# Kernel tuning notes

Measured on AMD Instinct MI355X. Metric: run time of the kernel, lower is better.

The kernel has to match this reference:

```python
import jax, jax.numpy as jnp
import numpy as np

DIM = 1024
HEADS = 16
HEAD_DIM = DIM // HEADS
FFN = 4 * DIM
EPS = 1e-5


def layer_norm(x, g, b):
    mu = jnp.mean(x, axis=-1, keepdims=True)
    var = jnp.mean(jnp.square(x - mu), axis=-1, keepdims=True)
    return (x - mu) * jax.lax.rsqrt(var + EPS) * g + b


def setup_inputs() -> dict:
    key = jax.random.key(0)
    ks = jax.random.split(key, 12)
    s_d = 1.0 / np.sqrt(DIM)
    s_f = 1.0 / np.sqrt(FFN)
    return {
        "x": jax.random.normal(ks[0], (2, 2048, DIM), dtype=jnp.float32),
        "ln1_g": jnp.ones((DIM,), jnp.float32),
        "ln1_b": jnp.zeros((DIM,), jnp.float32),
        "q_w": jax.random.normal(ks[1], (DIM, DIM), jnp.float32) * s_d,
        "k_w": jax.random.normal(ks[2], (DIM, DIM), jnp.float32) * s_d,
        "v_w": jax.random.normal(ks[3], (DIM, DIM), jnp.float32) * s_d,
        "o_w": jax.random.normal(ks[4], (DIM, DIM), jnp.float32) * s_d,
        "ln2_g": jnp.ones((DIM,), jnp.float32),
        "ln2_b": jnp.zeros((DIM,), jnp.float32),
        "ffn_in_w": jax.random.normal(ks[5], (FFN, DIM), jnp.float32) * s_d,
        "ffn_in_b": jnp.zeros((FFN,), jnp.float32),
        "sw_w": jax.random.normal(ks[6], (FFN, FFN), jnp.float32) * s_f,
        "sw_v": jax.random.normal(ks[7], (FFN, FFN), jnp.float32) * s_f,
        "ffn_out_w": jax.random.normal(ks[8], (DIM, FFN), jnp.float32) * s_f,
        "ffn_out_b": jnp.zeros((DIM,), jnp.float32),
    }


def reference(x, ln1_g, ln1_b, q_w, k_w, v_w, o_w, ln2_g, ln2_b,
              ffn_in_w, ffn_in_b, sw_w, sw_v, ffn_out_w, ffn_out_b):
    B, L, D = x.shape
    scale = HEAD_DIM ** -0.5

    # --- attention block ---
    h = layer_norm(x, ln1_g, ln1_b)
    q = (h @ q_w.T).reshape(B, L, HEADS, HEAD_DIM).transpose(0, 2, 1, 3)
    k = (h @ k_w.T).reshape(B, L, HEADS, HEAD_DIM).transpose(0, 2, 1, 3)
    v = (h @ v_w.T).reshape(B, L, HEADS, HEAD_DIM).transpose(0, 2, 1, 3)
    attn = jnp.einsum("bhqd,bhkd->bhqk", q, k) * scale
    attn = jax.nn.softmax(attn, axis=-1)
    out = jnp.einsum("bhqk,bhkd->bhqd", attn, v)
    out = out.transpose(0, 2, 1, 3).reshape(B, L, D)
    x = x + out @ o_w.T

    # --- FFN block: Linear -> SwiGLU -> Linear ---
    h = layer_norm(x, ln2_g, ln2_b)
    u = h @ ffn_in_w.T + ffn_in_b                 # [B,L,FFN]
    g = jax.nn.silu(u @ sw_w.T) * (u @ sw_v.T)    # SwiGLU
    x = x + g @ ffn_out_w.T + ffn_out_b
    return x
```

## Files before the change

kernel.cpp:

```cpp
#include <hip/hip_runtime.h>
#include <hip/hip_bf16.h>

#define TOK 4096
#define DIM 1024
#define FFN_N 4096
#define SEQ 2048
#define HD 64

using short8 = __attribute__((ext_vector_type(8))) short;
using short4v = __attribute__((ext_vector_type(4))) short;
using f32x4 = __attribute__((ext_vector_type(4))) float;

__device__ __forceinline__ short f2b(float f){
  return __builtin_bit_cast(short, __float2bfloat16(f));
}
__device__ __forceinline__ float b2f(short s){
  return __bfloat162float(__builtin_bit_cast(__hip_bfloat16, s));
}
__device__ __forceinline__ unsigned cvtpk(float lo, float hi){
  unsigned r;
  asm("v_cvt_pk_bf16_f32 %0, %1, %2" : "=v"(r) : "v"(lo), "v"(hi));
  return r;
}

__device__ __forceinline__ void gl_lds16(const short* g, short* l){
  __builtin_amdgcn_global_load_lds(
      (const __attribute__((address_space(1))) unsigned int*)g,
      (__attribute__((address_space(3))) unsigned int*)l, 16, 0, 0);
}

#define BARRAW() asm volatile("s_barrier" ::: "memory")
#define VMCNT(n) asm volatile("s_waitcnt vmcnt(" #n ")" ::: "memory")

__global__ __launch_bounds__(256) void castk(const float* __restrict__ src,
                                             short* __restrict__ dst, int n){
  int stride = gridDim.x*256*4;
  for (int i = (blockIdx.x*256 + threadIdx.x)*4; i < n; i += stride){
    float4 v = *reinterpret_cast<const float4*>(src + i);
    short4v o; o[0]=f2b(v.x); o[1]=f2b(v.y); o[2]=f2b(v.z); o[3]=f2b(v.w);
    *reinterpret_cast<short4v*>(dst + i) = o;
  }
}

__global__ __launch_bounds__(256) void lnk(const float* __restrict__ x,
                                           const float* __restrict__ g,
                                           const float* __restrict__ b,
                                           short* __restrict__ out){
  int row = blockIdx.x;
  int t = threadIdx.x;
  const float* xr = x + (size_t)row*DIM;
  float4 v = *reinterpret_cast<const float4*>(xr + t*4);
  float s = v.x+v.y+v.z+v.w;
  float s2 = v.x*v.x+v.y*v.y+v.z*v.z+v.w*v.w;
  #pragma unroll
  for (int off=1; off<64; off<<=1){ s += __shfl_xor(s,off); s2 += __shfl_xor(s2,off); }
  __shared__ float as_[4], as2_[4];
  if ((t&63)==0){ as_[t>>6]=s; as2_[t>>6]=s2; }
  __syncthreads();
  s = as_[0]+as_[1]+as_[2]+as_[3];
  s2 = as2_[0]+as2_[1]+as2_[2]+as2_[3];
  float mu = s * (1.0f/DIM);
  float var = s2 * (1.0f/DIM) - mu*mu;
  float r = rsqrtf(var + 1e-5f);
  float4 gv = *reinterpret_cast<const float4*>(g + t*4);
  float4 bv = *reinterpret_cast<const float4*>(b + t*4);
  short4v o;
  o[0]=f2b((v.x-mu)*r*gv.x + bv.x);
  o[1]=f2b((v.y-mu)*r*gv.y + bv.y);
  o[2]=f2b((v.z-mu)*r*gv.z + bv.z);
  o[3]=f2b((v.w-mu)*r*gv.w + bv.w);
  *reinterpret_cast<short4v*>(out + (size_t)row*DIM + t*4) = o;
}

template<int MODE>
__global__ __launch_bounds__(256,2) void gemm_bt(
    const short* __restrict__ A, const short* __restrict__ Bt,
    short* __restrict__ Cb, float* __restrict__ Cf,
    const float* __restrict__ bias, const float* __restrict__ resid,
    const short* __restrict__ aux,
    int M, int N, int K)
{
  __shared__ __align__(16) short Al[128*32];
  __shared__ __align__(16) short Bl[128*32];
  const int tid = threadIdx.x, lane = tid & 63, w = tid >> 6;
  const int wr = w >> 1, wc = w & 1;
  const int bx = blockIdx.x, by = blockIdx.y;

  const short* ga0 = A  + (size_t)(by*128 + w*32 + (lane>>2))*K + (lane&3)*8;
  const short* gb0 = Bt + (size_t)(bx*128 + w*32 + (lane>>2))*K + (lane&3)*8;
  short* la0 = &Al[w*32*32];
  short* lb0 = &Bl[w*32*32];

  f32x4 acc[4][4] = {};

  for (int k0 = 0; k0 < K; k0 += 32){
    __syncthreads();
    gl_lds16(ga0 + k0,                 la0);
    gl_lds16(ga0 + k0 + (size_t)16*K,  la0 + 16*32);
    gl_lds16(gb0 + k0,                 lb0);
    gl_lds16(gb0 + k0 + (size_t)16*K,  lb0 + 16*32);
    __syncthreads();
    short8 af[4], bf[4];
    #pragma unroll
    for (int m=0;m<4;m++)
      af[m] = *reinterpret_cast<const short8*>(&Al[(wr*64 + m*16 + (lane&15))*32 + (lane>>4)*8]);
    #pragma unroll
    for (int n=0;n<4;n++)
      bf[n] = *reinterpret_cast<const short8*>(&Bl[(wc*64 + n*16 + (lane&15))*32 + (lane>>4)*8]);
    #pragma unroll
    for (int m=0;m<4;m++)
      #pragma unroll
      for (int n=0;n<4;n++)
        acc[m][n] = __builtin_amdgcn_mfma_f32_16x16x32_bf16(af[m], bf[n], acc[m][n], 0,0,0);
  }

  #pragma unroll
  for (int m=0;m<4;m++){
    #pragma unroll
    for (int n=0;n<4;n++){
      #pragma unroll
      for (int j=0;j<4;j++){
        int r = by*128 + wr*64 + m*16 + ((lane>>4)<<2) + j;
        int c = bx*128 + wc*64 + n*16 + (lane&15);
        float v = acc[m][n][j];
        if (MODE==1 || MODE==3) v += bias[c];
        size_t idx = (size_t)r*N + c;
        if (MODE==4){
          float a = b2f(aux[idx]);
          float sg = a / (1.0f + __expf(-a));
          Cb[idx] = f2b(sg * v);
        } else if (MODE<=1) {
          Cb[idx] = f2b(v);
        } else {
          Cf[idx] = resid[idx] + v;
        }
      }
    }
  }
}

template<int MODE>
__global__ __launch_bounds__(512,2) void gemm256(
    const short* __restrict__ A, const short* __restrict__ Bt,
    short* __restrict__ Cb,
    const float* __restrict__ bias, const short* __restrict__ aux,
    int M, int N, int K)
{
  __shared__ __align__(16) short L[65536];
  const int tid = threadIdx.x, lane = tid&63, w = tid>>6;
  const int q15 = lane&15, h8 = lane>>4;
  const int wm = w>>2, wn = w&3;
  const int NT = K>>6;

  int bid = blockIdx.x;
  int wg = (bid&7)*(gridDim.x>>3) + (bid>>3);
  const int by = wg >> 4, bx = wg & 15;

  const int isub = w*8 + (lane>>3);
  const int koff = ((lane&7) ^ ((lane>>3)&7))*8;

  const short* gA[2][2]; const short* gB[2][2];
  #pragma unroll
  for (int hh=0; hh<2; hh++){
    #pragma unroll
    for (int j=0; j<2; j++){
      int i = j*64 + isub;
      int Ra = by*256 + (i>>6)*128 + hh*64 + (i&63);
      gA[hh][j] = A + (size_t)Ra*K + koff;
      int Rb = bx*256 + (i>>5)*64 + hh*32 + (i&31);
      gB[hh][j] = Bt + (size_t)Rb*K + koff;
    }
  }

  auto stA = [&](int db, int hh, int j, int kt){
    gl_lds16(gA[hh][j] + (size_t)kt*64, &L[db*32768 + hh*8192 + j*4096 + w*512]);
  };
  auto stB = [&](int db, int hh, int j, int kt){
    gl_lds16(gB[hh][j] + (size_t)kt*64, &L[db*32768 + (2+hh)*8192 + j*4096 + w*512]);
  };
  auto rdA = [&](int db, int mh, int m, int ks)->short8{
    int i = wm*64 + m*16 + q15;
    int ch = (ks*4 + h8) ^ (i&7);
    return *reinterpret_cast<const short8*>(&L[db*32768 + mh*8192 + i*64 + ch*8]);
  };
  auto rdB = [&](int db, int nh, int n, int ks)->short8{
    int i = wn*32 + n*16 + q15;
    int ch = (ks*4 + h8) ^ (i&7);
    return *reinterpret_cast<const short8*>(&L[db*32768 + (2+nh)*8192 + i*64 + ch*8]);
  };

  f32x4 acc[8][4] = {};
  short8 af[4][2], bf0[2][2], bf1[2][2];

#define MFMA_QUAD(MH, NH, BF)                                                  \
  __builtin_amdgcn_s_setprio(1);                                               \
  _Pragma("unroll")                                                            \
  for (int m=0;m<4;m++){                                                       \
    _Pragma("unroll")                                                          \
    for (int n=0;n<2;n++){                                                     \
      acc[(MH)*4+m][(NH)*2+n] = __builtin_amdgcn_mfma_f32_16x16x32_bf16(       \
          af[m][0], BF[n][0], acc[(MH)*4+m][(NH)*2+n], 0,0,0);                 \
      acc[(MH)*4+m][(NH)*2+n] = __builtin_amdgcn_mfma_f32_16x16x32_bf16(       \
          af[m][1], BF[n][1], acc[(MH)*4+m][(NH)*2+n], 0,0,0);                 \
    }                                                                          \
  }                                                                            \
  __builtin_amdgcn_s_setprio(0);

  stA(0,0,0,0); stA(0,0,1,0);
  stB(0,0,0,0); stB(0,0,1,0);
  stA(0,1,0,0); stA(0,1,1,0);
  stB(0,1,0,0); stB(0,1,1,0);
  VMCNT(4);
  BARRAW();

  for (int t = 0; t < NT; ++t){
    const int db = t&1;
    const bool pf = (t+1 < NT);

    #pragma unroll
    for (int m=0;m<4;m++){ af[m][0]=rdA(db,0,m,0); af[m][1]=rdA(db,0,m,1); }
    #pragma unroll
    for (int n=0;n<2;n++){ bf0[n][0]=rdB(db,0,n,0); bf0[n][1]=rdB(db,0,n,1); }
    if (pf){ stA(db^1,0,0,t+1); stA(db^1,0,1,t+1);
             stB(db^1,0,0,t+1); stB(db^1,0,1,t+1); }
    BARRAW();
    MFMA_QUAD(0,0,bf0);
    if (pf){ VMCNT(4); } else { VMCNT(0); }
    BARRAW();

    #pragma unroll
    for (int n=0;n<2;n++){ bf1[n][0]=rdB(db,1,n,0); bf1[n][1]=rdB(db,1,n,1); }
    if (pf){ stA(db^1,1,0,t+1); stA(db^1,1,1,t+1);
             stB(db^1,1,0,t+1); stB(db^1,1,1,t+1); }
    BARRAW();
    MFMA_QUAD(0,1,bf1);
    BARRAW();

    #pragma unroll
    for (int m=0;m<4;m++){ af[m][0]=rdA(db,1,m,0); af[m][1]=rdA(db,1,m,1); }
    BARRAW();
    MFMA_QUAD(1,1,bf1);
    BARRAW();

    BARRAW();
    MFMA_QUAD(1,0,bf0);
    if (pf){ VMCNT(4); } else { VMCNT(0); }
    BARRAW();
  }

  #pragma unroll
  for (int mq=0;mq<8;mq++){
    #pragma unroll
    for (int nq=0;nq<4;nq++){
      #pragma unroll
      for (int jj=0;jj<4;jj++){
        int r = by*256 + wm*128 + mq*16 + h8*4 + jj;
        int c = bx*256 + wn*64  + nq*16 + q15;
        float v = acc[mq][nq][jj];
        if (MODE==1) v += bias[c];
        size_t idx = (size_t)r*N + c;
        if (MODE==4){
          float a = b2f(aux[idx]);
          float sg = a / (1.0f + __expf(-a));
          Cb[idx] = f2b(sg * v);
        } else {
          Cb[idx] = f2b(v);
        }
      }
    }
  }
#undef MFMA_QUAD
}

__global__ __launch_bounds__(256) void vtrk(const short* __restrict__ V,
                                            short* __restrict__ Vt){
  __shared__ __align__(16) short T[64*72];
  const int tid = threadIdx.x;
  const int bh = blockIdx.y;
  const int b = bh >> 4, hd = bh & 15;
  const int t0 = blockIdx.x * 64;
  const short* src = V + (size_t)b*SEQ*DIM + (size_t)hd*HD;

  const int r = tid>>2, c = tid&3;
  short8 a0 = *reinterpret_cast<const short8*>(src + (size_t)(t0+r)*DIM + c*8);
  short8 a1 = *reinterpret_cast<const short8*>(src + (size_t)(t0+r)*DIM + (c+4)*8);
  *reinterpret_cast<short8*>(&T[r*72 + c*8]) = a0;
  *reinterpret_cast<short8*>(&T[r*72 + (c+4)*8]) = a1;
  __syncthreads();

  short* dst = Vt + (size_t)bh*HD*SEQ;
  #pragma unroll
  for (int dd=0; dd<2; dd++){
    int d = (tid>>3) + dd*32;
    int tc = tid&7;
    short8 o;
    #pragma unroll
    for (int j=0;j<8;j++) o[j] = T[(tc*8+j)*72 + d];
    *reinterpret_cast<short8*>(dst + (size_t)d*SEQ + t0 + tc*8) = o;
  }
}

__global__ __launch_bounds__(256) void attnk(
    const short* __restrict__ Q, const short* __restrict__ K,
    const short* __restrict__ Vt, short* __restrict__ O)
{
  __shared__ __align__(16) short Kl[64*64];
  __shared__ __align__(16) short Vl[64*64];
  __shared__ __align__(16) short Pl[4*16*72];

  const int tid = threadIdx.x, lane = tid&63, w = tid>>6;
  const int h = lane>>4, q15 = lane&15;
  const int bh = blockIdx.y;
  const int b = bh >> 4, hd = bh & 15;
  const int q0 = blockIdx.x * 64;
  const size_t base = (size_t)b*SEQ*DIM + (size_t)hd*HD;
  const size_t vbase = (size_t)bh*HD*SEQ;

  short8 aq[2];
  {
    int qrow = q0 + w*16 + q15;
    const short* qp = Q + base + (size_t)qrow*DIM + h*8;
    aq[0] = *reinterpret_cast<const short8*>(qp);
    aq[1] = *reinterpret_cast<const short8*>(qp + 32);
  }

  float mrun = -1e30f, lrun = 0.f;
  f32x4 o[4] = {};

  const int ksub = lane>>3;
  const int kchunk = (lane&7) ^ ksub;
  const short* kg0 = K + base + (size_t)(w*16 + ksub)*DIM + kchunk*8;
  const short* kg1 = kg0 + (size_t)8*DIM;
  const short* vg0 = Vt + vbase + (size_t)(w*16 + ksub)*SEQ + kchunk*8;
  const short* vg1 = vg0 + (size_t)8*SEQ;
  short* kl0 = &Kl[(w*16)*64];
  short* kl1 = &Kl[(w*16 + 8)*64];
  short* vl0 = &Vl[(w*16)*64];
  short* vl1 = &Vl[(w*16 + 8)*64];

  short* plw = &Pl[w*16*72];
  const int xk = (q15&7);

  for (int kv0 = 0; kv0 < SEQ; kv0 += 64){
    __syncthreads();
    gl_lds16(kg0 + (size_t)kv0*DIM, kl0);
    gl_lds16(kg1 + (size_t)kv0*DIM, kl1);
    gl_lds16(vg0 + kv0, vl0);
    gl_lds16(vg1 + kv0, vl1);
    __syncthreads();

    f32x4 s[4];
    #pragma unroll
    for (int nt=0; nt<4; nt++){
      const short8 kf0 = *reinterpret_cast<const short8*>(
          &Kl[(nt*16+q15)*64 + ((h    ^ xk)*8)]);
      const short8 kf1 = *reinterpret_cast<const short8*>(
          &Kl[(nt*16+q15)*64 + (((4+h)^ xk)*8)]);
      f32x4 t = {};
      t = __builtin_amdgcn_mfma_f32_16x16x32_bf16(kf0, aq[0], t, 0,0,0);
      t = __builtin_amdgcn_mfma_f32_16x16x32_bf16(kf1, aq[1], t, 0,0,0);
      s[nt] = t * 0.125f;
    }

    float pm = s[0][0];
    #pragma unroll
    for (int nt=0; nt<4; nt++)
      #pragma unroll
      for (int j=0; j<4; j++) pm = fmaxf(pm, s[nt][j]);
    pm = fmaxf(pm, __shfl_xor(pm, 16));
    pm = fmaxf(pm, __shfl_xor(pm, 32));

    float mn = fmaxf(mrun, pm);
    float al = __expf(mrun - mn);
    mrun = mn;
    float rs = 0.f;
    #pragma unroll
    for (int nt=0; nt<4; nt++)
      #pragma unroll
      for (int j=0; j<4; j++){
        s[nt][j] = __expf(s[nt][j] - mn);
        rs += s[nt][j];
      }
    rs += __shfl_xor(rs, 16);
    rs += __shfl_xor(rs, 32);
    lrun = lrun*al + rs;

    float alj[4];
    #pragma unroll
    for (int j=0;j<4;j++) alj[j] = __shfl(al, 4*h + j);
    #pragma unroll
    for (int dt=0;dt<4;dt++)
      #pragma unroll
      for (int j=0;j<4;j++) o[dt][j] *= alj[j];

    #pragma unroll
    for (int nt=0;nt<4;nt++){
      uint2 u;
      u.x = cvtpk(s[nt][0], s[nt][1]);
      u.y = cvtpk(s[nt][2], s[nt][3]);
      *reinterpret_cast<uint2*>(&plw[q15*72 + nt*16 + 4*h]) = u;
    }
    asm volatile("s_waitcnt lgkmcnt(0)" ::: "memory");
    const short8 ap0 = *reinterpret_cast<const short8*>(&plw[q15*72 +      h*8]);
    const short8 ap1 = *reinterpret_cast<const short8*>(&plw[q15*72 + 32 + h*8]);

    #pragma unroll
    for (int dt=0;dt<4;dt++){
      const short8 vf0 = *reinterpret_cast<const short8*>(
          &Vl[(dt*16+q15)*64 + ((h    ^ xk)*8)]);
      const short8 vf1 = *reinterpret_cast<const short8*>(
          &Vl[(dt*16+q15)*64 + (((4+h)^ xk)*8)]);
      o[dt] = __builtin_amdgcn_mfma_f32_16x16x32_bf16(ap0, vf0, o[dt], 0,0,0);
      o[dt] = __builtin_amdgcn_mfma_f32_16x16x32_bf16(ap1, vf1, o[dt], 0,0,0);
    }
  }

  float rl[4];
  #pragma unroll
  for (int j=0;j<4;j++) rl[j] = 1.0f / __shfl(lrun, 4*h + j);
  #pragma unroll
  for (int dt=0;dt<4;dt++)
    #pragma unroll
    for (int j=0;j<4;j++){
      int qrow = q0 + w*16 + 4*h + j;
      O[base + (size_t)qrow*DIM + dt*16 + q15] = f2b(o[dt][j]*rl[j]);
    }
}

extern "C" void kernel_launch(void* const* d_in, const int* in_sizes, int n_in,
                              void* d_out, int out_size, void* d_ws, size_t ws_size,
                              hipStream_t stream) {
  const float* x     = (const float*)d_in[0];
  const float* ln1_g = (const float*)d_in[1];
  const float* ln1_b = (const float*)d_in[2];
  const float* q_w   = (const float*)d_in[3];
  const float* k_w   = (const float*)d_in[4];
  const float* v_w   = (const float*)d_in[5];
  const float* o_w   = (const float*)d_in[6];
  const float* ln2_g = (const float*)d_in[7];
  const float* ln2_b = (const float*)d_in[8];
  const float* fi_w  = (const float*)d_in[9];
  const float* fi_b  = (const float*)d_in[10];
  const float* sw_w  = (const float*)d_in[11];
  const float* sw_v  = (const float*)d_in[12];
  const float* fo_w  = (const float*)d_in[13];
  const float* fo_b  = (const float*)d_in[14];
  float* out = (float*)d_out;

  char* W = (char*)d_ws;
  const size_t MB = 1024*1024;
  short* qw  = (short*)(W +   0*MB);
  short* kw  = (short*)(W +   2*MB);
  short* vw  = (short*)(W +   4*MB);
  short* ow  = (short*)(W +   6*MB);
  short* fiw = (short*)(W +   8*MB);
  short* sww = (short*)(W +  16*MB);
  short* swv = (short*)(W +  48*MB);
  short* fow = (short*)(W +  80*MB);
  short* hb  = (short*)(W +  88*MB);
  short* qb  = (short*)(W +  96*MB);
  short* kb  = (short*)(W + 104*MB);
  short* vb  = (short*)(W + 112*MB);
  short* ab  = (short*)(W + 120*MB);
  float* x2  = (float*)(W + 128*MB);
  short* ub  = (short*)(W + 144*MB);
  short* gb  = (short*)(W + 176*MB);
  short* a1  = (short*)(W +  96*MB);
  short* vt  = (short*)(W + 144*MB);

  dim3 blk(256);
  castk<<<1024,blk,0,stream>>>(q_w, qw, 1024*1024);
  castk<<<1024,blk,0,stream>>>(k_w, kw, 1024*1024);
  castk<<<1024,blk,0,stream>>>(v_w, vw, 1024*1024);
  castk<<<1024,blk,0,stream>>>(o_w, ow, 1024*1024);
  castk<<<2048,blk,0,stream>>>(fi_w, fiw, 4096*1024);
  castk<<<2048,blk,0,stream>>>(sw_w, sww, 4096*4096);
  castk<<<2048,blk,0,stream>>>(sw_v, swv, 4096*4096);
  castk<<<2048,blk,0,stream>>>(fo_w, fow, 1024*4096);

  lnk<<<TOK,blk,0,stream>>>(x, ln1_g, ln1_b, hb);
  gemm_bt<0><<<dim3(8,32),blk,0,stream>>>(hb, qw, qb, nullptr, nullptr, nullptr, nullptr, TOK, DIM, DIM);
  gemm_bt<0><<<dim3(8,32),blk,0,stream>>>(hb, kw, kb, nullptr, nullptr, nullptr, nullptr, TOK, DIM, DIM);
  gemm_bt<0><<<dim3(8,32),blk,0,stream>>>(hb, vw, vb, nullptr, nullptr, nullptr, nullptr, TOK, DIM, DIM);
  vtrk<<<dim3(SEQ/64,32),blk,0,stream>>>(vb, vt);
  attnk<<<dim3(32,32),blk,0,stream>>>(qb, kb, vt, ab);
  gemm_bt<2><<<dim3(8,32),blk,0,stream>>>(ab, ow, nullptr, x2, nullptr, x, nullptr, TOK, DIM, DIM);
  lnk<<<TOK,blk,0,stream>>>(x2, ln2_g, ln2_b, hb);
  gemm256<1><<<256, 512, 0, stream>>>(hb, fiw, ub, fi_b, nullptr, TOK, FFN_N, DIM);
  gemm256<0><<<256, 512, 0, stream>>>(ub, sww, a1, nullptr, nullptr, TOK, FFN_N, FFN_N);
  gemm256<4><<<256, 512, 0, stream>>>(ub, swv, gb, nullptr, a1, TOK, FFN_N, FFN_N);
  gemm_bt<3><<<dim3(8,32),blk,0,stream>>>(gb, fow, nullptr, out, fo_b, x2, nullptr, TOK, DIM, FFN_N);
}
```

Before: 647.4 us.

## Fuse Q/K/V projections into one GEMM and trim barriers in gemm256 loop

```diff
diff --git a/kernel.cpp b/kernel.cpp
--- a/kernel.cpp
+++ b/kernel.cpp
@@ -6,6 +6,7 @@
 #define FFN_N 4096
 #define SEQ 2048
 #define HD 64
+#define QKS 3072
 
 using short8 = __attribute__((ext_vector_type(8))) short;
 using short4v = __attribute__((ext_vector_type(4))) short;
@@ -223,8 +224,8 @@
     for (int n=0;n<2;n++){ bf0[n][0]=rdB(db,0,n,0); bf0[n][1]=rdB(db,0,n,1); }
     if (pf){ stA(db^1,0,0,t+1); stA(db^1,0,1,t+1);
              stB(db^1,0,0,t+1); stB(db^1,0,1,t+1); }
-    BARRAW();
     MFMA_QUAD(0,0,bf0);
+
     if (pf){ VMCNT(4); } else { VMCNT(0); }
     BARRAW();
 
@@ -232,19 +233,14 @@
     for (int n=0;n<2;n++){ bf1[n][0]=rdB(db,1,n,0); bf1[n][1]=rdB(db,1,n,1); }
     if (pf){ stA(db^1,1,0,t+1); stA(db^1,1,1,t+1);
              stB(db^1,1,0,t+1); stB(db^1,1,1,t+1); }
-    BARRAW();
     MFMA_QUAD(0,1,bf1);
-    BARRAW();
 
     #pragma unroll
     for (int m=0;m<4;m++){ af[m][0]=rdA(db,1,m,0); af[m][1]=rdA(db,1,m,1); }
-    BARRAW();
     MFMA_QUAD(1,1,bf1);
-    BARRAW();
-
-    BARRAW();
     MFMA_QUAD(1,0,bf0);
-    if (pf){ VMCNT(4); } else { VMCNT(0); }
+
+    if (pf){ VMCNT(4); }
     BARRAW();
   }
 
@@ -279,11 +275,11 @@
   const int bh = blockIdx.y;
   const int b = bh >> 4, hd = bh & 15;
   const int t0 = blockIdx.x * 64;
-  const short* src = V + (size_t)b*SEQ*DIM + (size_t)hd*HD;
+  const short* src = V + (size_t)b*SEQ*QKS + (size_t)hd*HD;
 
   const int r = tid>>2, c = tid&3;
-  short8 a0 = *reinterpret_cast<const short8*>(src + (size_t)(t0+r)*DIM + c*8);
-  short8 a1 = *reinterpret_cast<const short8*>(src + (size_t)(t0+r)*DIM + (c+4)*8);
+  short8 a0 = *reinterpret_cast<const short8*>(src + (size_t)(t0+r)*QKS + c*8);
+  short8 a1 = *reinterpret_cast<const short8*>(src + (size_t)(t0+r)*QKS + (c+4)*8);
   *reinterpret_cast<short8*>(&T[r*72 + c*8]) = a0;
   *reinterpret_cast<short8*>(&T[r*72 + (c+4)*8]) = a1;
   __syncthreads();
@@ -313,13 +309,14 @@
   const int bh = blockIdx.y;
   const int b = bh >> 4, hd = bh & 15;
   const int q0 = blockIdx.x * 64;
-  const size_t base = (size_t)b*SEQ*DIM + (size_t)hd*HD;
+  const size_t base  = (size_t)b*SEQ*QKS + (size_t)hd*HD;
+  const size_t obase = (size_t)b*SEQ*DIM + (size_t)hd*HD;
   const size_t vbase = (size_t)bh*HD*SEQ;
 
   short8 aq[2];
   {
     int qrow = q0 + w*16 + q15;
-    const short* qp = Q + base + (size_t)qrow*DIM + h*8;
+    const short* qp = Q + base + (size_t)qrow*QKS + h*8;
     aq[0] = *reinterpret_cast<const short8*>(qp);
     aq[1] = *reinterpret_cast<const short8*>(qp + 32);
   }
@@ -329,8 +326,8 @@
 
   const int ksub = lane>>3;
   const int kchunk = (lane&7) ^ ksub;
-  const short* kg0 = K + base + (size_t)(w*16 + ksub)*DIM + kchunk*8;
-  const short* kg1 = kg0 + (size_t)8*DIM;
+  const short* kg0 = K + base + (size_t)(w*16 + ksub)*QKS + kchunk*8;
+  const short* kg1 = kg0 + (size_t)8*QKS;
   const short* vg0 = Vt + vbase + (size_t)(w*16 + ksub)*SEQ + kchunk*8;
   const short* vg1 = vg0 + (size_t)8*SEQ;
   short* kl0 = &Kl[(w*16)*64];
@@ -343,8 +340,8 @@
 
   for (int kv0 = 0; kv0 < SEQ; kv0 += 64){
     __syncthreads();
-    gl_lds16(kg0 + (size_t)kv0*DIM, kl0);
-    gl_lds16(kg1 + (size_t)kv0*DIM, kl1);
+    gl_lds16(kg0 + (size_t)kv0*QKS, kl0);
+    gl_lds16(kg1 + (size_t)kv0*QKS, kl1);
     gl_lds16(vg0 + kv0, vl0);
     gl_lds16(vg1 + kv0, vl1);
     __syncthreads();
@@ -423,7 +420,7 @@
     #pragma unroll
     for (int j=0;j<4;j++){
       int qrow = q0 + w*16 + 4*h + j;
-      O[base + (size_t)qrow*DIM + dt*16 + q15] = f2b(o[dt][j]*rl[j]);
+      O[obase + (size_t)qrow*DIM + dt*16 + q15] = f2b(o[dt][j]*rl[j]);
     }
 }
 
@@ -449,29 +446,25 @@
 
   char* W = (char*)d_ws;
   const size_t MB = 1024*1024;
-  short* qw  = (short*)(W +   0*MB);
-  short* kw  = (short*)(W +   2*MB);
-  short* vw  = (short*)(W +   4*MB);
-  short* ow  = (short*)(W +   6*MB);
-  short* fiw = (short*)(W +   8*MB);
-  short* sww = (short*)(W +  16*MB);
-  short* swv = (short*)(W +  48*MB);
-  short* fow = (short*)(W +  80*MB);
-  short* hb  = (short*)(W +  88*MB);
-  short* qb  = (short*)(W +  96*MB);
-  short* kb  = (short*)(W + 104*MB);
-  short* vb  = (short*)(W + 112*MB);
-  short* ab  = (short*)(W + 120*MB);
-  float* x2  = (float*)(W + 128*MB);
-  short* ub  = (short*)(W + 144*MB);
-  short* gb  = (short*)(W + 176*MB);
-  short* a1  = (short*)(W +  96*MB);
-  short* vt  = (short*)(W + 144*MB);
+  short* qkvw = (short*)(W +   0*MB);
+  short* ow   = (short*)(W +   6*MB);
+  short* fiw  = (short*)(W +   8*MB);
+  short* sww  = (short*)(W +  16*MB);
+  short* swv  = (short*)(W +  48*MB);
+  short* fow  = (short*)(W +  80*MB);
+  short* hb   = (short*)(W +  88*MB);
+  short* qkv  = (short*)(W +  96*MB);
+  short* ab   = (short*)(W + 120*MB);
+  float* x2   = (float*)(W + 128*MB);
+  short* ub   = (short*)(W + 144*MB);
+  short* gb   = (short*)(W + 176*MB);
+  short* a1   = (short*)(W +  96*MB);
+  short* vt   = (short*)(W + 144*MB);
 
   dim3 blk(256);
-  castk<<<1024,blk,0,stream>>>(q_w, qw, 1024*1024);
-  castk<<<1024,blk,0,stream>>>(k_w, kw, 1024*1024);
-  castk<<<1024,blk,0,stream>>>(v_w, vw, 1024*1024);
+  castk<<<1024,blk,0,stream>>>(q_w, qkvw,             1024*1024);
+  castk<<<1024,blk,0,stream>>>(k_w, qkvw + 1024*1024, 1024*1024);
+  castk<<<1024,blk,0,stream>>>(v_w, qkvw + 2048*1024, 1024*1024);
   castk<<<1024,blk,0,stream>>>(o_w, ow, 1024*1024);
   castk<<<2048,blk,0,stream>>>(fi_w, fiw, 4096*1024);
   castk<<<2048,blk,0,stream>>>(sw_w, sww, 4096*4096);
@@ -479,11 +472,9 @@
   castk<<<2048,blk,0,stream>>>(fo_w, fow, 1024*4096);
 
   lnk<<<TOK,blk,0,stream>>>(x, ln1_g, ln1_b, hb);
-  gemm_bt<0><<<dim3(8,32),blk,0,stream>>>(hb, qw, qb, nullptr, nullptr, nullptr, nullptr, TOK, DIM, DIM);
-  gemm_bt<0><<<dim3(8,32),blk,0,stream>>>(hb, kw, kb, nullptr, nullptr, nullptr, nullptr, TOK, DIM, DIM);
-  gemm_bt<0><<<dim3(8,32),blk,0,stream>>>(hb, vw, vb, nullptr, nullptr, nullptr, nullptr, TOK, DIM, DIM);
-  vtrk<<<dim3(SEQ/64,32),blk,0,stream>>>(vb, vt);
-  attnk<<<dim3(32,32),blk,0,stream>>>(qb, kb, vt, ab);
+  gemm_bt<0><<<dim3(24,32),blk,0,stream>>>(hb, qkvw, qkv, nullptr, nullptr, nullptr, nullptr, TOK, QKS, DIM);
+  vtrk<<<dim3(SEQ/64,32),blk,0,stream>>>(qkv + 2048, vt);
+  attnk<<<dim3(32,32),blk,0,stream>>>(qkv, qkv + 1024, vt, ab);
   gemm_bt<2><<<dim3(8,32),blk,0,stream>>>(ab, ow, nullptr, x2, nullptr, x, nullptr, TOK, DIM, DIM);
   lnk<<<TOK,blk,0,stream>>>(x2, ln2_g, ln2_b, hb);
   gemm256<1><<<256, 512, 0, stream>>>(hb, fiw, ub, fi_b, nullptr, TOK, FFN_N, DIM);
```

New measurement: 574.4 us. -11.3%, faster.
